# Optimization experiments

Measured on AMD Instinct MI355X. Metric: run time of the kernel, lower is better.

## Reference

```python
import jax, jax.numpy as jnp
import numpy as np

EPS_ANGLE = 1e-8   # eps in _cos_angle's F.normalize
EPS_NORM = 1e-12   # default F.normalize eps used for the similarity matrix
TOPK = 4
EXTRA_FRAMES = (1, 3, 5, 7)          # teacher-only frames
SHARED_TEACHER = (2, 4, 6)           # shared frames in teacher indexing
SHARED_STUDENT = (1, 2, 3)           # same frames in student indexing
W1 = W2 = W3 = 1.0


def _angle_cosines(ref, shared, sim):
    """Cosines of the 3 RKD angles for every (ref r, shared s, sim k) triplet.
    ref: [B,R,D], shared: [B,S,D], sim: [B,R,K,D]. Returns 3 arrays [B,R,S,K].
    Uses the dot-product expansion (u-v).(w-v) = uw - uv - vw + vv so the
    [B,R,S,K,D] difference tensors are never materialized (same math as the
    chunked torch loop)."""
    rr = jnp.sum(ref * ref, -1)                       # [B,R]
    ss = jnp.sum(shared * shared, -1)                 # [B,S]
    hh = jnp.sum(sim * sim, -1)                       # [B,R,K]
    sr = jnp.einsum('brd,bsd->brs', ref, shared)      # [B,R,S]
    rh = jnp.einsum('brd,brkd->brk', ref, sim)        # [B,R,K]
    sh = jnp.einsum('bsd,brkd->brsk', shared, sim)    # [B,R,S,K]
    rr_ = rr[:, :, None, None]
    ss_ = ss[:, None, :, None]
    hh_ = hh[:, :, None, :]
    sr_ = sr[..., None]
    rh_ = rh[:, :, None, :]
    n_sr = jnp.sqrt(jnp.maximum(ss_ - 2 * sr_ + rr_, 0.0))  # ||shared-ref||
    n_hr = jnp.sqrt(jnp.maximum(hh_ - 2 * rh_ + rr_, 0.0))  # ||sim-ref||
    n_sh = jnp.sqrt(jnp.maximum(ss_ - 2 * sh + hh_, 0.0))   # ||shared-sim||
    cl = lambda n: jnp.maximum(n, EPS_ANGLE)
    a1 = (sh - rh_ - sr_ + rr_) / (cl(n_sr) * cl(n_hr))  # angle at ref
    a2 = (sr_ - sh - rh_ + hh_) / (cl(n_hr) * cl(n_sh))  # angle at sim
    a3 = (rh_ - sr_ - sh + ss_) / (cl(n_sr) * cl(n_sh))  # angle at shared
    return a1, a2, a3


def _l2n(x, eps):
    return x / jnp.maximum(jnp.linalg.norm(x, axis=-1, keepdims=True), eps)


def setup_inputs() -> dict:
    key = jax.random.key(0)
    k1, k2, k3, k4 = jax.random.split(key, 4)
    B, P, D = 4, 1024, 1024
    return {
        'teacher_feats': jax.random.normal(k1, (B, 8, P, D), dtype=jnp.float32),
        'student_feats': jax.random.normal(k2, (B, 4, P, D), dtype=jnp.float32),
        'ref_perm': jax.random.randint(k3, (256,), 0, P),
        'shared_perm': jax.random.randint(k4, (256,), 0, P),
    }


def reference(teacher_feats, student_feats, ref_perm, shared_perm):
    B, St, P, D = teacher_feats.shape
    R = ref_perm.shape[0]
    S = shared_perm.shape[0]
    sg = jax.lax.stop_gradient

    ref_t = sg(teacher_feats[:, 0, ref_perm, :])        # [B,R,D]
    ref_s = student_feats[:, 0, ref_perm, :]            # [B,R,D]

    # teacher-only (extra) frames, concatenated along patch dim -> [B,4P,D]
    extra_t = sg(teacher_feats[:, jnp.array(EXTRA_FRAMES), :, :]).reshape(B, len(EXTRA_FRAMES) * P, D)
    sim = jnp.einsum('brd,bed->bre', _l2n(ref_t, EPS_NORM), _l2n(extra_t, EPS_NORM))
    _, topk_idx = jax.lax.top_k(sim, TOPK)              # [B,R,K]
    sim_high = jax.vmap(lambda e, i: e[i])(extra_t, topk_idx)  # [B,R,K,D]
    sim_high = sg(sim_high)

    s1 = s2 = s3 = jnp.float32(0.0)
    for ti, si in zip(SHARED_TEACHER, SHARED_STUDENT):
        sh_t = sg(teacher_feats[:, ti, shared_perm, :])
        sh_s = student_feats[:, si, shared_perm, :]
        a1t, a2t, a3t = _angle_cosines(ref_t, sh_t, sim_high)
        a1s, a2s, a3s = _angle_cosines(ref_s, sh_s, sim_high)
        s1 = s1 + jnp.sum(jnp.abs(a1s - sg(a1t)))
        s2 = s2 + jnp.sum(jnp.abs(a2s - sg(a2t)))
        s3 = s3 + jnp.sum(jnp.abs(a3s - sg(a3t)))

    total_elements = len(SHARED_TEACHER) * B * R * S * TOPK
    loss = (W1 * s1 + W2 * s2 + W3 * s3) / total_elements
    return loss
```

## Files before the change

kernel.cpp:

```cpp
#include <hip/hip_runtime.h>
#include <float.h>

#define BB 4
#define PP 1024
#define DD 1024
#define RR 256
#define SSZ 256
#define KT 4
#define EE 4096
#define NPAIR 3

typedef float  f32x4  __attribute__((ext_vector_type(4)));
typedef short  short8 __attribute__((ext_vector_type(8)));

#define MFMA16(a,b,c) __builtin_amdgcn_mfma_f32_16x16x32_bf16((a),(b),(c),0,0,0)
#define GLOAD_LDS(g, l) __builtin_amdgcn_global_load_lds( \
    (const __attribute__((address_space(1))) void*)(g),   \
    (__attribute__((address_space(3))) void*)(l), 16, 0, 0)

#define OFF_NE    ((size_t)0)
#define OFF_RR_T  ((size_t)16384)
#define OFF_RR_S  ((size_t)17408)
#define OFF_HH    ((size_t)18432)
#define OFF_RH_T  ((size_t)22528)
#define OFF_RH_S  ((size_t)26624)
#define OFF_SS_T  ((size_t)30720)
#define OFF_SS_S  ((size_t)33792)
#define OFF_TOPK  ((size_t)36864)
#define OFF_ACC   ((size_t)40960)
#define OFF_CAND  ((size_t)45056)
#define FLOAT_END ((size_t)569344)

#define U_REF_T ((size_t)0)
#define U_REF_S ((size_t)2097152)
#define U_SIMH  ((size_t)4194304)
#define U_SH_T  ((size_t)8388608)
#define U_SH_S  ((size_t)11534336)
#define U_EXT   ((size_t)14680064)

__device__ inline float block_sum256(float v, float* sb) {
  v += __shfl_down(v, 32); v += __shfl_down(v, 16);
  v += __shfl_down(v, 8);  v += __shfl_down(v, 4);
  v += __shfl_down(v, 2);  v += __shfl_down(v, 1);
  int lane = threadIdx.x & 63, wid = threadIdx.x >> 6;
  if (lane == 0) sb[wid] = v;
  __syncthreads();
  float r = 0.f;
  if (threadIdx.x < 4) r = sb[threadIdx.x];
  r += __shfl_down(r, 2); r += __shfl_down(r, 1);
  __syncthreads();
  return r;
}

__device__ inline float dot4(const float4& a, const float4& b) {
  return a.x*b.x + a.y*b.y + a.z*b.z + a.w*b.w;
}

__device__ inline unsigned short bhi(float x) {
  unsigned u = __float_as_uint(x);
  return (unsigned short)((u + 0x7fffu + ((u >> 16) & 1u)) >> 16);
}
__device__ inline ushort4 h4of(float4 f) {
  return make_ushort4(bhi(f.x), bhi(f.y), bhi(f.z), bhi(f.w));
}

__device__ inline size_t wofs(size_t base, int R, int t) {
  int rr = R & 15;
  int ss = ((t >> 1) & 3) ^ ((rr >> 1) & 3);
  return base + (size_t)(R >> 4)*16384 + (size_t)(t >> 3)*512
       + rr*32 + ss*8 + (t & 1)*4;
}

__global__ __launch_bounds__(256) void k_prep(const float* __restrict__ T,
                                              const float* __restrict__ Sf,
                                              const int* __restrict__ ref_perm,
                                              const int* __restrict__ shared_perm,
                                              float* __restrict__ ws) {
  __shared__ float sb[4];
  ushort* uws = (ushort*)(ws + FLOAT_END);
  int blk = blockIdx.x;
  int t = threadIdx.x;
  if (blk < 1024) {
    int b = blk >> 8, r = blk & 255;
    int pos = ref_perm[r];
    const float4* ts = (const float4*)(T  + ((size_t)(b*8 + 0)*PP + pos)*DD);
    const float4* sv = (const float4*)(Sf + ((size_t)(b*4 + 0)*PP + pos)*DD);
    float4 a = ts[t], c = sv[t];
    int R = b*RR + r;
    *(ushort4*)(uws + wofs(U_REF_T, R, t)) = h4of(a);
    *(ushort4*)(uws + wofs(U_REF_S, R, t)) = h4of(c);
    float r1 = block_sum256(dot4(a, a), sb);
    float r2 = block_sum256(dot4(c, c), sb);
    if (t == 0) {
      ws[OFF_RR_T + R] = r1;
      ws[OFF_RR_S + R] = r2;
    }
  } else if (blk < 17408) {
    int i = blk - 1024;
    int b = i >> 12, e = i & 4095;
    int f = 1 + 2*(e >> 10);
    int pos = e & 1023;
    const float4* src = (const float4*)(T + ((size_t)(b*8 + f)*PP + pos)*DD);
    float4 a = src[t];
    *(ushort4*)(uws + wofs(U_EXT, b*EE + e, t)) = h4of(a);
    float tot = block_sum256(dot4(a, a), sb);
    if (t == 0) ws[OFF_NE + (size_t)b*EE + e] = fmaxf(sqrtf(tot), 1e-12f);
  } else {
    int idx = blk - 17408;
    int p = idx / (BB*SSZ);
    int b = (idx / SSZ) % BB;
    int s = idx % SSZ;
    int pos = shared_perm[s];
    int ti = 2*(p + 1), si = p + 1;
    const float4* tr = (const float4*)(T  + ((size_t)(b*8 + ti)*PP + pos)*DD);
    const float4* sr = (const float4*)(Sf + ((size_t)(b*4 + si)*PP + pos)*DD);
    float4 a = tr[t], c = sr[t];
    *(ushort4*)(uws + wofs(U_SH_T, idx, t)) = h4of(a);
    *(ushort4*)(uws + wofs(U_SH_S, idx, t)) = h4of(c);
    float r1 = block_sum256(dot4(a, a), sb);
    float r2 = block_sum256(dot4(c, c), sb);
    if (t == 0) { ws[OFF_SS_T + idx] = r1; ws[OFF_SS_S + idx] = r2; }
  }
}

__global__ __launch_bounds__(512, 8) void k_sim(float* __restrict__ ws) {
  __shared__ union SM {
    ushort stg[2][128][32];
    float simv[64][68];
  } sm;
  const ushort* uws = (const ushort*)(ws + FLOAT_END);
  int d = blockIdx.x;
  int u8 = d & 7, q = d >> 3;
  int e_t = q >> 1, r_loc = q & 1;
  int b = u8 >> 1, rhalf = u8 & 1;
  int e0 = e_t * 64;
  int r0 = (rhalf*2 + r_loc) * 64;
  int tid = threadIdx.x;
  int w = tid >> 6, lane = tid & 63;
  int l15 = tid & 15, lq = (tid >> 4) & 3;
  int af = w & 3, b2 = w >> 2;

  const ushort* gsrc;
  if (w < 4) gsrc = uws + U_REF_T + ((size_t)((b*RR + r0) >> 4) + w)*16384 + lane*8;
  else       gsrc = uws + U_EXT   + ((size_t)((b*EE + e0) >> 4) + (w - 4))*16384 + lane*8;

  f32x4 acc[2];
  acc[0] = (f32x4){0.f, 0.f, 0.f, 0.f};
  acc[1] = (f32x4){0.f, 0.f, 0.f, 0.f};

  GLOAD_LDS(gsrc, &sm.stg[0][16*w][0]);
  gsrc += 512;

  int cur = 0;
#pragma unroll 1
  for (int k0 = 0; k0 < 32; ++k0) {
    if (k0 < 31) {
      GLOAD_LDS(gsrc, &sm.stg[cur ^ 1][16*w][0]);
      gsrc += 512;
      asm volatile("s_waitcnt vmcnt(1)" ::: "memory");
    } else {
      asm volatile("s_waitcnt vmcnt(0)" ::: "memory");
    }
    __builtin_amdgcn_s_barrier();
    __builtin_amdgcn_sched_barrier(0);
    int rtA = af*16 + l15;
    short8 ah = *(const short8*)&sm.stg[cur][rtA][(lq ^ ((rtA >> 1) & 3))*8];
#pragma unroll
    for (int j = 0; j < 2; ++j) {
      int rtB = 64 + (b2*2 + j)*16 + l15;
      short8 bh = *(const short8*)&sm.stg[cur][rtB][(lq ^ ((rtB >> 1) & 3))*8];
      acc[j] = MFMA16(ah, bh, acc[j]);
    }
    __builtin_amdgcn_sched_barrier(0);
    __builtin_amdgcn_s_barrier();
    cur ^= 1;
  }

  float invs[2];
#pragma unroll
  for (int j = 0; j < 2; ++j)
    invs[j] = 1.f / ws[OFF_NE + (size_t)b*EE + e0 + (b2*2 + j)*16 + l15];
  __syncthreads();
#pragma unroll
  for (int j = 0; j < 2; ++j) {
    int e_loc = (b2*2 + j)*16 + l15;
#pragma unroll
    for (int q2 = 0; q2 < 4; ++q2)
      sm.simv[af*16 + lq*4 + q2][e_loc] = acc[j][q2] * invs[j];
  }
  __syncthreads();
  if (tid < 64) {
    float v[4] = {-FLT_MAX, -FLT_MAX, -FLT_MAX, -FLT_MAX};
    int ix[4] = {0x7fffffff, 0x7fffffff, 0x7fffffff, 0x7fffffff};
#pragma unroll 1
    for (int e = 0; e < 64; ++e) {
      float f = sm.simv[tid][e];
      if (f > v[3]) {
        int eg = e0 + e;
        if (f > v[0])      { v[3]=v[2]; ix[3]=ix[2]; v[2]=v[1]; ix[2]=ix[1]; v[1]=v[0]; ix[1]=ix[0]; v[0]=f; ix[0]=eg; }
        else if (f > v[1]) { v[3]=v[2]; ix[3]=ix[2]; v[2]=v[1]; ix[2]=ix[1]; v[1]=f; ix[1]=eg; }
        else if (f > v[2]) { v[3]=v[2]; ix[3]=ix[2]; v[2]=f; ix[2]=eg; }
        else               { v[3]=f; ix[3]=eg; }
      }
    }
    float2* cand = (float2*)(ws + OFF_CAND);
    size_t base = (((size_t)(b*RR + r0 + tid))*64 + e_t)*4;
#pragma unroll
    for (int k = 0; k < 4; ++k)
      cand[base + k] = make_float2(v[k], __int_as_float(ix[k]));
  }
}

__global__ __launch_bounds__(256) void k_topk2(float* __restrict__ ws) {
  __shared__ float rv[256];
  __shared__ int   ri[256];
  __shared__ int   winIdx;
  int br = blockIdx.x;
  int tid = threadIdx.x;
  const float2* cand = (const float2*)(ws + OFF_CAND);
  float2 c = cand[(size_t)br*256 + tid];
  float v = c.x;
  int idx = __float_as_int(c.y);
  int* outi = (int*)(ws + OFF_TOPK) + (size_t)br*KT;
  for (int k = 0; k < KT; ++k) {
    rv[tid] = v; ri[tid] = idx;
    __syncthreads();
    for (int off = 128; off > 0; off >>= 1) {
      if (tid < off) {
        float v2 = rv[tid+off]; int i2 = ri[tid+off];
        if (v2 > rv[tid] || (v2 == rv[tid] && i2 < ri[tid])) { rv[tid] = v2; ri[tid] = i2; }
      }
      __syncthreads();
    }
    if (tid == 0) { outi[k] = ri[0]; winIdx = ri[0]; }
    __syncthreads();
    if (idx == winIdx) v = -FLT_MAX;
    __syncthreads();
  }
}

__global__ __launch_bounds__(256) void k_gather_high(const float* __restrict__ T,
                                                     const float* __restrict__ Sf,
                                                     const int* __restrict__ ref_perm,
                                                     float* __restrict__ ws) {
  __shared__ float sb[4];
  int idx = blockIdx.x;
  int e = ((const int*)(ws + OFF_TOPK))[idx];
  int b = idx >> 10;
  int r = (idx >> 2) & 255;
  int rpos = ref_perm[r];
  const float4* src = (const float4*)(T + ((size_t)(b*8 + 1 + 2*(e >> 10))*PP + (e & 1023))*DD);
  const float4* rt  = (const float4*)(T  + ((size_t)(b*8 + 0)*PP + rpos)*DD);
  const float4* rs  = (const float4*)(Sf + ((size_t)(b*4 + 0)*PP + rpos)*DD);
  ushort* uws = (ushort*)(ws + FLOAT_END);
  int t = threadIdx.x;
  float4 h = src[t];
  *(ushort4*)(uws + wofs(U_SIMH, idx, t)) = h4of(h);
  float4 a = rt[t], c = rs[t];
  float r1 = block_sum256(dot4(h, h), sb);
  float r2 = block_sum256(dot4(h, a), sb);
  float r3 = block_sum256(dot4(h, c), sb);
  if (t == 0) { ws[OFF_HH + idx] = r1; ws[OFF_RH_T + idx] = r2; ws[OFF_RH_S + idx] = r3; }
}

__global__ __launch_bounds__(256) void k_main(float* __restrict__ ws,
                                              double* __restrict__ acc_out) {
  __shared__ float Ct[4][80][17];
  __shared__ float Cs2[4][80][17];
  __shared__ float sb[4];
  const ushort* uws = (const ushort*)(ws + FLOAT_END);

  int d = blockIdx.x;
  int u8 = d & 7, q = d >> 3;
  int b = u8 >> 1, rhalf = u8 & 1;
  int p = q >> 5;
  int rem = q & 31;
  int s16 = rem >> 1, rq = rem & 1;
  int tid = threadIdx.x;
  int w = tid >> 6, lane = tid & 63;
  int z = p*4 + b;
  int r16i = rhalf*8 + rq*4 + w;
  int r0 = r16i*16, s0 = s16*16;

  int l15 = lane & 15, lq = (lane >> 4) & 3;
  int laneoff = l15*32 + ((lq ^ ((l15 >> 1) & 3)))*8;

  const ushort* pa0; const ushort* pa1; const ushort* pa2; const ushort* pa3;
  const ushort* prt; const ushort* prs; const ushort* pbt; const ushort* pbs;
  {
    size_t gs = (size_t)((b*RR + r0) >> 2);
    pa0 = uws + U_SIMH + (gs + 0)*16384 + laneoff;
    pa1 = uws + U_SIMH + (gs + 1)*16384 + laneoff;
    pa2 = uws + U_SIMH + (gs + 2)*16384 + laneoff;
    pa3 = uws + U_SIMH + (gs + 3)*16384 + laneoff;
    size_t gr = (size_t)((b*RR + r0) >> 4);
    prt = uws + U_REF_T + gr*16384 + laneoff;
    prs = uws + U_REF_S + gr*16384 + laneoff;
    size_t gh = (size_t)((z*SSZ + s0) >> 4);
    pbt = uws + U_SH_T + gh*16384 + laneoff;
    pbs = uws + U_SH_S + gh*16384 + laneoff;
  }

  f32x4 aT0, aT1, aT2, aT3, aRT, aS0, aS1, aS2, aS3, aRS;
  aT0 = aT1 = aT2 = aT3 = aRT = aS0 = aS1 = aS2 = aS3 = aRS = (f32x4){0.f,0.f,0.f,0.f};

#pragma unroll 4
  for (int c = 0; c < 32; ++c) {
    int o = c*512;
    short8 bt = *(const short8*)(pbt + o);
    short8 bs = *(const short8*)(pbs + o);
    short8 a0 = *(const short8*)(pa0 + o);
    short8 a1 = *(const short8*)(pa1 + o);
    short8 a2 = *(const short8*)(pa2 + o);
    short8 a3 = *(const short8*)(pa3 + o);
    short8 rt = *(const short8*)(prt + o);
    short8 rs = *(const short8*)(prs + o);
    aT0 = MFMA16(a0, bt, aT0);
    aT1 = MFMA16(a1, bt, aT1);
    aT2 = MFMA16(a2, bt, aT2);
    aT3 = MFMA16(a3, bt, aT3);
    aRT = MFMA16(rt, bt, aRT);
    aS0 = MFMA16(a0, bs, aS0);
    aS1 = MFMA16(a1, bs, aS1);
    aS2 = MFMA16(a2, bs, aS2);
    aS3 = MFMA16(a3, bs, aS3);
    aRS = MFMA16(rs, bs, aRS);
  }

#pragma unroll
  for (int q2 = 0; q2 < 4; ++q2) {
    int rg = lq*4 + q2;
    Ct[w][ 0 + rg][l15] = aT0[q2];
    Ct[w][16 + rg][l15] = aT1[q2];
    Ct[w][32 + rg][l15] = aT2[q2];
    Ct[w][48 + rg][l15] = aT3[q2];
    Ct[w][64 + rg][l15] = aRT[q2];
    Cs2[w][ 0 + rg][l15] = aS0[q2];
    Cs2[w][16 + rg][l15] = aS1[q2];
    Cs2[w][32 + rg][l15] = aS2[q2];
    Cs2[w][48 + rg][l15] = aS3[q2];
    Cs2[w][64 + rg][l15] = aRS[q2];
  }
  __syncthreads();

  int rl = lane >> 2, sg = lane & 3;
  int r = r0 + rl;
  float rrt = ws[OFF_RR_T + b*RR + r];
  float rrs = ws[OFF_RR_S + b*RR + r];
  float hhk[4], rhtk[4], rhsk[4], ihr_t[4], ihr_s[4];
#pragma unroll
  for (int k = 0; k < 4; ++k) {
    int idx = (b*RR + r)*KT + k;
    hhk[k]  = ws[OFF_HH + idx];
    rhtk[k] = ws[OFF_RH_T + idx];
    rhsk[k] = ws[OFF_RH_S + idx];
    float nt = sqrtf(fmaxf(hhk[k] - 2.f*rhtk[k] + rrt, 0.f));
    float ns = sqrtf(fmaxf(hhk[k] - 2.f*rhsk[k] + rrs, 0.f));
    ihr_t[k] = 1.f / fmaxf(nt, 1e-8f);
    ihr_s[k] = 1.f / fmaxf(ns, 1e-8f);
  }
  float local = 0.f;
#pragma unroll
  for (int j = 0; j < 4; ++j) {
    int sl = sg*4 + j;
    int sidx = z*SSZ + s0 + sl;
    float sst = ws[OFF_SS_T + sidx];
    float sss = ws[OFF_SS_S + sidx];
    float srt = Ct[w][64 + rl][sl];
    float srs = Cs2[w][64 + rl][sl];
    float isr_t = 1.f / fmaxf(sqrtf(fmaxf(sst - 2.f*srt + rrt, 0.f)), 1e-8f);
    float isr_s = 1.f / fmaxf(sqrtf(fmaxf(sss - 2.f*srs + rrs, 0.f)), 1e-8f);
#pragma unroll
    for (int k = 0; k < 4; ++k) {
      float sht = Ct[w][rl*4 + k][sl];
      float shs = Cs2[w][rl*4 + k][sl];
      float ish_t = 1.f / fmaxf(sqrtf(fmaxf(sst - 2.f*sht + hhk[k], 0.f)), 1e-8f);
      float ish_s = 1.f / fmaxf(sqrtf(fmaxf(sss - 2.f*shs + hhk[k], 0.f)), 1e-8f);
      float a1t = (sht - rhtk[k] - srt + rrt) * (isr_t * ihr_t[k]);
      float a2t = (srt - sht - rhtk[k] + hhk[k]) * (ihr_t[k] * ish_t);
      float a3t = (rhtk[k] - srt - sht + sst) * (isr_t * ish_t);
      float a1s = (shs - rhsk[k] - srs + rrs) * (isr_s * ihr_s[k]);
      float a2s = (srs - shs - rhsk[k] + hhk[k]) * (ihr_s[k] * ish_s);
      float a3s = (rhsk[k] - srs - shs + sss) * (isr_s * ish_s);
      local += fabsf(a1s - a1t) + fabsf(a2s - a2t) + fabsf(a3s - a3t);
    }
  }
  float tot = block_sum256(local, sb);
  if (tid == 0) atomicAdd(acc_out, (double)tot);
}

__global__ void k_final(const double* __restrict__ acc, float* __restrict__ out) {
  out[0] = (float)(acc[0] / 3145728.0);
}

extern "C" void kernel_launch(void* const* d_in, const int* in_sizes, int n_in,
                              void* d_out, int out_size, void* d_ws, size_t ws_size,
                              hipStream_t stream) {
  const float* T  = (const float*)d_in[0];
  const float* Sf = (const float*)d_in[1];
  const int* ref_perm    = (const int*)d_in[2];
  const int* shared_perm = (const int*)d_in[3];
  float* ws = (float*)d_ws;
  double* acc = (double*)(ws + OFF_ACC);

  hipMemsetAsync(acc, 0, sizeof(double), stream);
  k_prep<<<20480, 256, 0, stream>>>(T, Sf, ref_perm, shared_perm, ws);
  k_sim<<<1024, 512, 0, stream>>>(ws);
  k_topk2<<<BB*RR, 256, 0, stream>>>(ws);
  k_gather_high<<<BB*RR*KT, 256, 0, stream>>>(T, Sf, ref_perm, ws);
  k_main<<<768, 256, 0, stream>>>(ws, acc);
  k_final<<<1, 1, 0, stream>>>(acc, (float*)d_out);
}
```

Baseline: 146.3 us.

## Replace LDS-staged k_sim GEMM with direct register loads per wave

The similarity GEMM kernel drops its double-buffered global-to-LDS staging and barriers. Each wave now loads its own 16-row A tile and four 16-column B tiles straight from the pre-swizzled bf16 workspace into registers and runs four MFMAs per k-step. The block shrinks to 256 threads and does a per-wave top-4 with no block-level syncs. This removes barrier and LDS traffic, but the B tiles are no longer shared between waves, so more data is read from global memory and cache.

```diff
diff --git a/kernel.cpp b/kernel.cpp
--- a/kernel.cpp
+++ b/kernel.cpp
@@ -14,9 +14,6 @@
 typedef short  short8 __attribute__((ext_vector_type(8)));
 
 #define MFMA16(a,b,c) __builtin_amdgcn_mfma_f32_16x16x32_bf16((a),(b),(c),0,0,0)
-#define GLOAD_LDS(g, l) __builtin_amdgcn_global_load_lds( \
-    (const __attribute__((address_space(1))) void*)(g),   \
-    (__attribute__((address_space(3))) void*)(l), 16, 0, 0)
 
 #define OFF_NE    ((size_t)0)
 #define OFF_RR_T  ((size_t)16384)
@@ -123,78 +120,60 @@
   }
 }
 
-__global__ __launch_bounds__(512, 8) void k_sim(float* __restrict__ ws) {
-  __shared__ union SM {
-    ushort stg[2][128][32];
-    float simv[64][68];
-  } sm;
+__global__ __launch_bounds__(256) void k_sim(float* __restrict__ ws) {
+  __shared__ float simv[4][16][68];
   const ushort* uws = (const ushort*)(ws + FLOAT_END);
   int d = blockIdx.x;
   int u8 = d & 7, q = d >> 3;
-  int e_t = q >> 1, r_loc = q & 1;
-  int b = u8 >> 1, rhalf = u8 & 1;
-  int e0 = e_t * 64;
-  int r0 = (rhalf*2 + r_loc) * 64;
+  int b = u8 >> 1, eh = u8 & 1;
+  int eb = eh*32 + (q >> 2);
+  int rgq = q & 3;
   int tid = threadIdx.x;
   int w = tid >> 6, lane = tid & 63;
-  int l15 = tid & 15, lq = (tid >> 4) & 3;
-  int af = w & 3, b2 = w >> 2;
-
-  const ushort* gsrc;
-  if (w < 4) gsrc = uws + U_REF_T + ((size_t)((b*RR + r0) >> 4) + w)*16384 + lane*8;
-  else       gsrc = uws + U_EXT   + ((size_t)((b*EE + e0) >> 4) + (w - 4))*16384 + lane*8;
-
-  f32x4 acc[2];
-  acc[0] = (f32x4){0.f, 0.f, 0.f, 0.f};
-  acc[1] = (f32x4){0.f, 0.f, 0.f, 0.f};
-
-  GLOAD_LDS(gsrc, &sm.stg[0][16*w][0]);
-  gsrc += 512;
-
-  int cur = 0;
-#pragma unroll 1
-  for (int k0 = 0; k0 < 32; ++k0) {
-    if (k0 < 31) {
-      GLOAD_LDS(gsrc, &sm.stg[cur ^ 1][16*w][0]);
-      gsrc += 512;
-      asm volatile("s_waitcnt vmcnt(1)" ::: "memory");
-    } else {
-      asm volatile("s_waitcnt vmcnt(0)" ::: "memory");
-    }
-    __builtin_amdgcn_s_barrier();
-    __builtin_amdgcn_sched_barrier(0);
-    int rtA = af*16 + l15;
-    short8 ah = *(const short8*)&sm.stg[cur][rtA][(lq ^ ((rtA >> 1) & 3))*8];
-#pragma unroll
-    for (int j = 0; j < 2; ++j) {
-      int rtB = 64 + (b2*2 + j)*16 + l15;
-      short8 bh = *(const short8*)&sm.stg[cur][rtB][(lq ^ ((rtB >> 1) & 3))*8];
-      acc[j] = MFMA16(ah, bh, acc[j]);
-    }
-    __builtin_amdgcn_sched_barrier(0);
-    __builtin_amdgcn_s_barrier();
-    cur ^= 1;
-  }
-
-  float invs[2];
-#pragma unroll
-  for (int j = 0; j < 2; ++j)
-    invs[j] = 1.f / ws[OFF_NE + (size_t)b*EE + e0 + (b2*2 + j)*16 + l15];
-  __syncthreads();
-#pragma unroll
-  for (int j = 0; j < 2; ++j) {
-    int e_loc = (b2*2 + j)*16 + l15;
+  int rg = rgq*4 + w;
+  int r0 = rg*16, e0 = eb*64;
+  int l15 = lane & 15, lq = (lane >> 4) & 3;
+  int laneoff = l15*32 + ((lq ^ ((l15 >> 1) & 3)))*8;
+
+  const ushort* pA = uws + U_REF_T + ((size_t)((b*RR + r0) >> 4))*16384 + laneoff;
+  const ushort* pB0 = uws + U_EXT + ((size_t)((b*EE + e0) >> 4) + 0)*16384 + laneoff;
+  const ushort* pB1 = uws + U_EXT + ((size_t)((b*EE + e0) >> 4) + 1)*16384 + laneoff;
+  const ushort* pB2 = uws + U_EXT + ((size_t)((b*EE + e0) >> 4) + 2)*16384 + laneoff;
+  const ushort* pB3 = uws + U_EXT + ((size_t)((b*EE + e0) >> 4) + 3)*16384 + laneoff;
+
+  f32x4 acc[4];
+#pragma unroll
+  for (int j = 0; j < 4; ++j) acc[j] = (f32x4){0.f, 0.f, 0.f, 0.f};
+
+#pragma unroll 4
+  for (int c = 0; c < 32; ++c) {
+    int o = c*512;
+    short8 ah = *(const short8*)(pA + o);
+    short8 b0 = *(const short8*)(pB0 + o);
+    short8 b1 = *(const short8*)(pB1 + o);
+    short8 b2 = *(const short8*)(pB2 + o);
+    short8 b3 = *(const short8*)(pB3 + o);
+    acc[0] = MFMA16(ah, b0, acc[0]);
+    acc[1] = MFMA16(ah, b1, acc[1]);
+    acc[2] = MFMA16(ah, b2, acc[2]);
+    acc[3] = MFMA16(ah, b3, acc[3]);
+  }
+
+  float invs[4];
+#pragma unroll
+  for (int j = 0; j < 4; ++j)
+    invs[j] = 1.f / ws[OFF_NE + (size_t)b*EE + e0 + j*16 + l15];
+#pragma unroll
+  for (int j = 0; j < 4; ++j)
 #pragma unroll
     for (int q2 = 0; q2 < 4; ++q2)
-      sm.simv[af*16 + lq*4 + q2][e_loc] = acc[j][q2] * invs[j];
-  }
-  __syncthreads();
-  if (tid < 64) {
+      simv[w][lq*4 + q2][j*16 + l15] = acc[j][q2] * invs[j];
+  if (lane < 16) {
     float v[4] = {-FLT_MAX, -FLT_MAX, -FLT_MAX, -FLT_MAX};
     int ix[4] = {0x7fffffff, 0x7fffffff, 0x7fffffff, 0x7fffffff};
 #pragma unroll 1
     for (int e = 0; e < 64; ++e) {
-      float f = sm.simv[tid][e];
+      float f = simv[w][lane][e];
       if (f > v[3]) {
         int eg = e0 + e;
         if (f > v[0])      { v[3]=v[2]; ix[3]=ix[2]; v[2]=v[1]; ix[2]=ix[1]; v[1]=v[0]; ix[1]=ix[0]; v[0]=f; ix[0]=eg; }
@@ -204,7 +183,7 @@
       }
     }
     float2* cand = (float2*)(ws + OFF_CAND);
-    size_t base = (((size_t)(b*RR + r0 + tid))*64 + e_t)*4;
+    size_t base = (((size_t)(b*RR + r0 + lane))*64 + eb)*4;
 #pragma unroll
     for (int k = 0; k < 4; ++k)
       cand[base + k] = make_float2(v[k], __int_as_float(ix[k]));
@@ -405,7 +384,7 @@
 
   hipMemsetAsync(acc, 0, sizeof(double), stream);
   k_prep<<<20480, 256, 0, stream>>>(T, Sf, ref_perm, shared_perm, ws);
-  k_sim<<<1024, 512, 0, stream>>>(ws);
+  k_sim<<<1024, 256, 0, stream>>>(ws);
   k_topk2<<<BB*RR, 256, 0, stream>>>(ws);
   k_gather_high<<<BB*RR*KT, 256, 0, stream>>>(T, Sf, ref_perm, ws);
   k_main<<<768, 256, 0, stream>>>(ws, acc);
```

Result: faster. 123.0 us (-16.0%).
